# Kernel tuning notes

Hardware: AMD Instinct MI355X
Metric: run time of the kernel (lower is better)

The kernel has to match this reference:

```python
import jax, jax.numpy as jnp
import numpy as np

B, T, D_IN, D_H1, D_H2, K = 8, 1024, 256, 1024, 1024, 9
EPS = 1e-12

def setup_inputs() -> dict:
    key = jax.random.key(0)
    ks = jax.random.split(key, 11)
    return {
        "x": jax.random.normal(ks[0], (B, T, D_IN), jnp.float32),
        "d_w": jax.random.normal(ks[1], (B, D_H1, 1, K), jnp.float32),
        "d_g": jax.random.uniform(ks[2], (B, D_H1), jnp.float32),
        "d_b": jax.random.normal(ks[3], (B, D_H1), jnp.float32) * 0.02,
        "p_w": jax.random.normal(ks[4], (B, D_H1, D_H2, 1), jnp.float32),
        "p_g": jax.random.uniform(ks[5], (B, D_H1), jnp.float32),
        "p_b": jax.random.normal(ks[6], (B, D_H2), jnp.float32) * 0.02,
        "w1_w": jax.random.normal(ks[7], (D_H1, D_IN), jnp.float32) / np.sqrt(D_IN),
        "w1_b": jnp.zeros((D_H1,), jnp.float32),
        "w2_w": jax.random.normal(ks[8], (D_IN, D_H2), jnp.float32) / np.sqrt(D_H2),
        "w2_b": jnp.zeros((D_IN,), jnp.float32),
    }

def _mish(v):
    return v * jnp.tanh(jax.nn.softplus(v))

def _wnorm(w, g):
    # F.normalize over channel dim 1, scaled by per-(batch,channel) gain g
    n = jnp.maximum(jnp.linalg.norm(w, axis=1, keepdims=True), EPS)
    return (w / n) * g[:, :, None, None]

def reference(x, d_w, d_g, d_b, p_w, p_g, p_b, w1_w, w1_b, w2_w, w2_b):
    residual = x
    # w_1: conv1x1 projection d_in -> d_hid1, channels-first [B, C, T]
    h = jnp.einsum('bti,ci->bct', x, w1_w) + w1_b[None, :, None]
    h = _mish(h)  # dropout is identity in eval
    k = d_w.shape[-1]
    p = (k - 1) // 2
    t = h.shape[-1]
    hp = jnp.pad(h, ((0, 0), (0, 0), (p, p)))
    # unfold: overlapping windows [B, C, T, K] (small fixed K loop)
    x_unf = jnp.stack([hp[:, :, i:i + t] for i in range(k)], axis=-1)
    dw = _wnorm(d_w, d_g)[:, :, 0, :]  # [B, C, K]
    y = jnp.einsum('bctk,bck->bct', x_unf, dw) + d_b[:, :, None]
    pw = _wnorm(p_w, p_g)[..., 0]      # [B, C, O]
    y = jnp.einsum('bct,bco->bot', y, pw) + p_b[:, :, None]
    # w_2: conv1x1 projection d_hid2 -> d_in, back to [B, T, d_in]
    out = jnp.einsum('bot,io->bti', y, w2_w) + w2_b
    return out + residual
```

## Files before the change

kernel.cpp:

```cpp
#include <hip/hip_runtime.h>
#include <hip/hip_bf16.h>

#define B_  8
#define T_  1024
#define DI_ 256
#define C_  1024
#define O_  1024
#define KW  9
#define BT_ 8192
#define EPSF 1e-12f

typedef unsigned short u16;
typedef u16   ushort8 __attribute__((ext_vector_type(8)));
typedef u16   ushort4v __attribute__((ext_vector_type(4)));
typedef __bf16 bf16x8 __attribute__((ext_vector_type(8)));
typedef float  f32x4  __attribute__((ext_vector_type(4)));

#define GLOAD_LDS16(g, l) __builtin_amdgcn_global_load_lds( \
    (const __attribute__((address_space(1))) void*)(g),      \
    (__attribute__((address_space(3))) void*)(l), 16, 0, 0)

__device__ __forceinline__ float bf2f(u16 u) {
    union { unsigned int i; float f; } z; z.i = ((unsigned int)u) << 16; return z.f;
}
__device__ __forceinline__ u16 f2bf(float f) {
    union { float f; unsigned int i; } z; z.f = f;
    unsigned int i = z.i;
    i += 0x7FFFu + ((i >> 16) & 1u);
    return (u16)(i >> 16);
}
__device__ __forceinline__ float mishf(float v) {
    float u = __expf(v);
    float w = 1.f + u;
    return v * (1.f - 2.f / (w * w + 1.f));
}

#define PB_XB 2048
#define PB_W1 2304
#define PB_W2 2560
#define PB_DN 2568
#define PB_PT 4616

__global__ __launch_bounds__(256)
void prep_k(const float* __restrict__ x,   u16* __restrict__ xb,
            const float* __restrict__ w1w, u16* __restrict__ w1b16,
            const float* __restrict__ w2w, u16* __restrict__ w2b16,
            const float* __restrict__ d_w, const float* __restrict__ d_g,
            float* __restrict__ dwf,
            const float* __restrict__ p_w, const float* __restrict__ p_g,
            float* __restrict__ part, u16* __restrict__ pwT)
{
    const int bid = blockIdx.x;
    const int tid = threadIdx.x;

    if (bid < PB_W2) {
        const float* in;
        u16* out;
        int i;
        if (bid < PB_XB)      { in = x;   out = xb;    i = bid * 256 + tid; }
        else if (bid < PB_W1) { in = w1w; out = w1b16; i = (bid - PB_XB) * 256 + tid; }
        else                  { in = w2w; out = w2b16; i = (bid - PB_W1) * 256 + tid; }
        float4 v = ((const float4*)in)[i];
        ushort4v o;
        o.x = f2bf(v.x); o.y = f2bf(v.y); o.z = f2bf(v.z); o.w = f2bf(v.w);
        ((ushort4v*)out)[i] = o;
    } else if (bid < PB_DN) {
        __shared__ float red[KW][256];
        __shared__ float nrm[KW];
        const int b = bid - PB_W2;
        float s[KW];
#pragma unroll
        for (int k = 0; k < KW; k++) s[k] = 0.f;
        for (int c = tid; c < C_; c += 256) {
#pragma unroll
            for (int k = 0; k < KW; k++) {
                float v = d_w[((size_t)b * C_ + c) * KW + k];
                s[k] += v * v;
            }
        }
#pragma unroll
        for (int k = 0; k < KW; k++) red[k][tid] = s[k];
        __syncthreads();
        if (tid < KW) {
            float t = 0.f;
            for (int i = 0; i < 256; i++) t += red[tid][i];
            nrm[tid] = fmaxf(sqrtf(t), EPSF);
        }
        __syncthreads();
        for (int c = tid; c < C_; c += 256) {
            float g = d_g[(size_t)b * C_ + c];
#pragma unroll
            for (int k = 0; k < KW; k++)
                dwf[((size_t)b * C_ + c) * KW + k] =
                    d_w[((size_t)b * C_ + c) * KW + k] / nrm[k] * g;
        }
    } else {
        __shared__ float ts[64][65];
        __shared__ float sq[4][64];
        const int idx = bid - PB_DN;
        const int b   = idx >> 8;
        const int rem = idx & 255;
        const int c0  = (rem >> 4) * 64, o0 = (rem & 15) * 64;
        const int col = tid & 63;
        const int rg  = tid >> 6;
        float ssq = 0.f;
        for (int r = rg; r < 64; r += 4) {
            float v = p_w[((size_t)b * C_ + c0 + r) * O_ + o0 + col];
            ssq += v * v;
            ts[r][col] = v * p_g[(size_t)b * C_ + c0 + r];
        }
        sq[rg][col] = ssq;
        __syncthreads();
        if (tid < 64)
            part[((size_t)b * 16 + (rem >> 4)) * O_ + o0 + tid] =
                sq[0][tid] + sq[1][tid] + sq[2][tid] + sq[3][tid];
        for (int r = rg; r < 64; r += 4)
            pwT[((size_t)b * O_ + o0 + r) * C_ + c0 + col] = f2bf(ts[col][r]);
    }
}

__global__ __launch_bounds__(256)
void dwconv_k(const u16* __restrict__ h, const float* __restrict__ dwf,
              const float* __restrict__ d_b, u16* __restrict__ y1gT)
{
    __shared__ u16 hs[64][74];
    const int b  = blockIdx.z;
    const int c0 = blockIdx.y * 64, t0 = blockIdx.x * 64;
    const int tid = threadIdx.x;
    for (int idx = tid; idx < 64 * 72; idx += 256) {
        int cc = idx / 72, tt = idx % 72;
        int t = t0 + tt - 4;
        u16 v = 0;
        if (t >= 0 && t < T_) v = h[(size_t)(c0 + cc) * BT_ + b * T_ + t];
        hs[cc][tt] = v;
    }
    __syncthreads();
    const int cc = tid & 63;
    const int c  = c0 + cc;
    float w[KW];
#pragma unroll
    for (int k = 0; k < KW; k++) w[k] = dwf[((size_t)b * C_ + c) * KW + k];
    const float bb = d_b[(size_t)b * C_ + c];
    for (int tt = tid >> 6; tt < 64; tt += 4) {
        float s = bb;
#pragma unroll
        for (int k = 0; k < KW; k++) s += bf2f(hs[cc][tt + k]) * w[k];
        y1gT[((size_t)b * T_ + t0 + tt) * C_ + c] = f2bf(s);
    }
}

template<int EPI>
__device__ __forceinline__ void gemmw_body(
    const u16* __restrict__ A, const u16* __restrict__ Bt,
    u16* __restrict__ Db, const float* __restrict__ bias,
    const float* __restrict__ extra, int M, int N, int Kd)
{
    __shared__ u16 As[2][128 * 32];
    __shared__ u16 Bs[2][256 * 32];

    const int gx = gridDim.x;
    const unsigned nwg = (unsigned)gx * gridDim.y;
    unsigned lin = blockIdx.y * gx + blockIdx.x;
    lin = (lin & 7u) * (nwg >> 3) + (lin >> 3);
    const int m0 = (int)(lin / gx) * 128;
    const int n0 = (int)(lin % gx) * 256;

    const int b = (EPI == 1) ? (m0 >> 10) : 0;
    if (EPI == 1) {
        Bt    += (size_t)b * O_ * C_;
        bias  += (size_t)b * O_;
        extra += (size_t)b * 16 * O_;
    }

    const int tid  = threadIdx.x;
    const int lane = tid & 63, wave = tid >> 6;
    const int wm = (wave >> 1) * 64, wn = (wave & 1) * 128;
    const int lr = lane & 15;

    const int srow  = lane >> 2;
    const int scolE = ((lane & 3) ^ (srow & 3)) * 8;

    f32x4 acc[4][8];
#pragma unroll
    for (int i = 0; i < 4; i++)
#pragma unroll
        for (int j = 0; j < 8; j++) acc[i][j] = (f32x4){0.f, 0.f, 0.f, 0.f};

    auto STAGE = [&](int buf, int k0) {
#pragma unroll
        for (int i = 0; i < 2; i++)
            GLOAD_LDS16(&A[(size_t)(m0 + i * 64 + wave * 16 + srow) * Kd + k0 + scolE],
                        &As[buf][(i * 64 + wave * 16) * 32]);
#pragma unroll
        for (int i = 0; i < 4; i++)
            GLOAD_LDS16(&Bt[(size_t)(n0 + i * 64 + wave * 16 + srow) * Kd + k0 + scolE],
                        &Bs[buf][(i * 64 + wave * 16) * 32]);
    };

    const int NT = Kd >> 5;
    STAGE(0, 0);
    for (int kt = 0; kt < NT; kt++) {
        __syncthreads();
        if (kt + 1 < NT) STAGE((kt + 1) & 1, (kt + 1) << 5);
        const u16* as = As[kt & 1];
        const u16* bs = Bs[kt & 1];
        const int slot = lane >> 4;
        const int sw = (slot ^ (lr & 3)) << 3;
        bf16x8 av[4], bv[8];
#pragma unroll
        for (int i = 0; i < 4; i++)
            av[i] = *(const bf16x8*)&as[(wm + i * 16 + lr) * 32 + sw];
#pragma unroll
        for (int j = 0; j < 8; j++)
            bv[j] = *(const bf16x8*)&bs[(wn + j * 16 + lr) * 32 + sw];
#pragma unroll
        for (int i = 0; i < 4; i++)
#pragma unroll
            for (int j = 0; j < 8; j++)
                acc[i][j] = __builtin_amdgcn_mfma_f32_16x16x32_bf16(
                    av[i], bv[j], acc[i][j], 0, 0, 0);
    }

    const int r0 = (lane >> 4) * 4;
#pragma unroll
    for (int i = 0; i < 4; i++) {
#pragma unroll
        for (int j = 0; j < 8; j++) {
            const int col = n0 + wn + j * 16 + lr;
            float iv = 0.f;
            if (EPI == 1) {
                float s = 0.f;
#pragma unroll
                for (int ch = 0; ch < 16; ch++)
                    s += extra[(size_t)ch * O_ + col];
                iv = 1.f / fmaxf(sqrtf(s), EPSF);
            }
#pragma unroll
            for (int r = 0; r < 4; r++) {
                const int row = m0 + wm + i * 16 + r0 + r;
                float v = acc[i][j][r];
                if (EPI == 0) {
                    v += bias[row];
                    v = mishf(v);
                } else {
                    v = v * iv + bias[col];
                }
                Db[(size_t)row * N + col] = f2bf(v);
            }
        }
    }
}

__global__ __launch_bounds__(256, 1)
void gemm1_k(const u16* __restrict__ A, const u16* __restrict__ Bt,
             u16* __restrict__ D, const float* __restrict__ bias,
             int M, int N, int Kd)
{
    gemmw_body<0>(A, Bt, D, bias, nullptr, M, N, Kd);
}

__global__ __launch_bounds__(256, 1)
void gemm2_k(const u16* __restrict__ A, const u16* __restrict__ Bt,
             u16* __restrict__ D, const float* __restrict__ bias,
             const float* __restrict__ extra, int M, int N, int Kd)
{
    gemmw_body<1>(A, Bt, D, bias, extra, M, N, Kd);
}

__global__ __launch_bounds__(256)
void gemm3_k(const u16* __restrict__ A, const u16* __restrict__ Bt,
             float* __restrict__ Df, const float* __restrict__ bias,
             const float* __restrict__ X, int M, int N, int Kd)
{
    __shared__ u16 As[2][128 * 64];
    __shared__ u16 Bs[2][64 * 64];

    const int gx = gridDim.x;
    const unsigned nwg = (unsigned)gx * gridDim.y;
    unsigned lin = blockIdx.y * gx + blockIdx.x;
    lin = (lin & 7u) * (nwg >> 3) + (lin >> 3);
    const int m0 = (int)(lin / gx) * 128;
    const int n0 = (int)(lin % gx) * 64;

    const int tid  = threadIdx.x;
    const int lane = tid & 63, wave = tid >> 6;
    const int wm = (wave & 1) * 64, wn = (wave >> 1) * 32;
    const int lr = lane & 15;

    const int sbase = wave * 8;
    const int srowL = lane >> 3;
    const int scolE = ((lane & 7) ^ srowL) * 8;

    f32x4 acc[4][2];
#pragma unroll
    for (int i = 0; i < 4; i++)
#pragma unroll
        for (int j = 0; j < 2; j++) acc[i][j] = (f32x4){0.f, 0.f, 0.f, 0.f};

    auto STAGE = [&](int buf, int k0) {
#pragma unroll
        for (int i = 0; i < 4; i++)
            GLOAD_LDS16(&A[(size_t)(m0 + i * 32 + sbase + srowL) * Kd + k0 + scolE],
                        &As[buf][(i * 32 + sbase) * 64]);
#pragma unroll
        for (int i = 0; i < 2; i++)
            GLOAD_LDS16(&Bt[(size_t)(n0 + i * 32 + sbase + srowL) * Kd + k0 + scolE],
                        &Bs[buf][(i * 32 + sbase) * 64]);
    };

    const int NT = Kd >> 6;
    STAGE(0, 0);
    for (int kt = 0; kt < NT; kt++) {
        __syncthreads();
        if (kt + 1 < NT) STAGE((kt + 1) & 1, (kt + 1) << 6);
        const u16* as = As[kt & 1];
        const u16* bs = Bs[kt & 1];
        bf16x8 av[2][4], bv[2][2];
#pragma unroll
        for (int kk = 0; kk < 2; kk++) {
            const int slot = (lane >> 4) + kk * 4;
            const int sw = (slot ^ (lr & 7)) << 3;
#pragma unroll
            for (int i = 0; i < 4; i++)
                av[kk][i] = *(const bf16x8*)&as[(wm + i * 16 + lr) * 64 + sw];
#pragma unroll
            for (int j = 0; j < 2; j++)
                bv[kk][j] = *(const bf16x8*)&bs[(wn + j * 16 + lr) * 64 + sw];
        }
#pragma unroll
        for (int kk = 0; kk < 2; kk++)
#pragma unroll
            for (int i = 0; i < 4; i++)
#pragma unroll
                for (int j = 0; j < 2; j++)
                    acc[i][j] = __builtin_amdgcn_mfma_f32_16x16x32_bf16(
                        av[kk][i], bv[kk][j], acc[i][j], 0, 0, 0);
    }

    const int r0 = (lane >> 4) * 4;
#pragma unroll
    for (int i = 0; i < 4; i++) {
#pragma unroll
        for (int j = 0; j < 2; j++) {
            const int col = n0 + wn + j * 16 + lr;
#pragma unroll
            for (int r = 0; r < 4; r++) {
                const int row = m0 + wm + i * 16 + r0 + r;
                Df[(size_t)row * N + col] =
                    acc[i][j][r] + bias[col] + X[(size_t)row * N + col];
            }
        }
    }
}

extern "C" void kernel_launch(void* const* d_in, const int* in_sizes, int n_in,
                              void* d_out, int out_size, void* d_ws, size_t ws_size,
                              hipStream_t stream)
{
    const float* x   = (const float*)d_in[0];
    const float* d_w = (const float*)d_in[1];
    const float* d_g = (const float*)d_in[2];
    const float* d_b = (const float*)d_in[3];
    const float* p_w = (const float*)d_in[4];
    const float* p_g = (const float*)d_in[5];
    const float* p_b = (const float*)d_in[6];
    const float* w1w = (const float*)d_in[7];
    const float* w1b = (const float*)d_in[8];
    const float* w2w = (const float*)d_in[9];
    const float* w2b = (const float*)d_in[10];
    float* out = (float*)d_out;

    char* ws = (char*)d_ws;
    const size_t SZ = (size_t)16777216;
    u16*   h    = (u16*)(ws);
    u16*   y1gT = (u16*)(ws + SZ);
    u16*   pwT  = (u16*)(ws + 2 * SZ);
    u16*   y2T  = (u16*)(ws + 3 * SZ);
    u16*   xb   = (u16*)(ws + 4 * SZ);
    u16*   w1b16= (u16*)(ws + 4 * SZ + 4194304);
    u16*   w2b16= (u16*)(ws + 4 * SZ + 4718592);
    float* dwf  = (float*)(ws + 4 * SZ + 5242880);
    float* part = (float*)(ws + 4 * SZ + 5242880 + 294912);

    prep_k<<<dim3(PB_PT), 256, 0, stream>>>(
        x, xb, w1w, w1b16, w2w, w2b16, d_w, d_g, dwf, p_w, p_g, part, pwT);

    gemm1_k<<<dim3(BT_ / 256, C_ / 128), 256, 0, stream>>>(
        w1b16, xb, h, w1b, C_, BT_, DI_);

    dwconv_k<<<dim3(T_ / 64, C_ / 64, B_), 256, 0, stream>>>(h, dwf, d_b, y1gT);

    gemm2_k<<<dim3(O_ / 256, BT_ / 128), 256, 0, stream>>>(
        y1gT, pwT, y2T, p_b, part, BT_, O_, C_);

    gemm3_k<<<dim3(DI_ / 64, BT_ / 128), 256, 0, stream>>>(
        y2T, w2b16, out, w2b, x, BT_, DI_, O_);
}
```

Measured before the change: 119.0 us.

## Triple-buffer GEMM pipelines with 8-wave tiles and smaller gemm3 blocks

The two large GEMMs (w1 projection and pointwise conv) move from 4 waves per 128x256 tile with a double-buffered K=32 stage to 8 waves with a triple-buffered K=64 stage. The per-iteration __syncthreads is replaced by a partial vmcnt wait plus s_barrier, and MFMA blocks are wrapped in s_setprio so load latency overlaps compute. The final GEMM shrinks to 64x64 tiles on 2 waves with triple-buffered K=32 stages, which raises block count and occupancy. This costs more LDS per block (144 KB for gemm1/2, from 48 KB) and relies on hand-counted vmcnt values being correct.

```diff
diff --git a/kernel.cpp b/kernel.cpp
--- a/kernel.cpp
+++ b/kernel.cpp
@@ -150,13 +150,13 @@
 }
 
 template<int EPI>
-__device__ __forceinline__ void gemmw_body(
+__device__ __forceinline__ void gemm12_body(
     const u16* __restrict__ A, const u16* __restrict__ Bt,
     u16* __restrict__ Db, const float* __restrict__ bias,
     const float* __restrict__ extra, int M, int N, int Kd)
 {
-    __shared__ u16 As[2][128 * 32];
-    __shared__ u16 Bs[2][256 * 32];
+    __shared__ u16 As[3 * 128 * 64];
+    __shared__ u16 Bs[3 * 256 * 64];
 
     const int gx = gridDim.x;
     const unsigned nwg = (unsigned)gx * gridDim.y;
@@ -174,58 +174,74 @@
 
     const int tid  = threadIdx.x;
     const int lane = tid & 63, wave = tid >> 6;
-    const int wm = (wave >> 1) * 64, wn = (wave & 1) * 128;
+    const int wm = (wave >> 2) * 64, wn = (wave & 3) * 64;
     const int lr = lane & 15;
-
-    const int srow  = lane >> 2;
-    const int scolE = ((lane & 3) ^ (srow & 3)) * 8;
-
-    f32x4 acc[4][8];
+    const int srow8 = tid >> 3;
+    const int scolE = ((tid & 7) ^ ((tid >> 3) & 7)) * 8;
+
+    f32x4 acc[4][4];
 #pragma unroll
     for (int i = 0; i < 4; i++)
 #pragma unroll
-        for (int j = 0; j < 8; j++) acc[i][j] = (f32x4){0.f, 0.f, 0.f, 0.f};
-
-    auto STAGE = [&](int buf, int k0) {
+        for (int j = 0; j < 4; j++) acc[i][j] = (f32x4){0.f, 0.f, 0.f, 0.f};
+
+    auto STAGE = [&](int buf, int kt) {
+        const int k0 = kt << 6;
 #pragma unroll
         for (int i = 0; i < 2; i++)
-            GLOAD_LDS16(&A[(size_t)(m0 + i * 64 + wave * 16 + srow) * Kd + k0 + scolE],
-                        &As[buf][(i * 64 + wave * 16) * 32]);
+            GLOAD_LDS16(&A[(size_t)(m0 + i * 64 + srow8) * Kd + k0 + scolE],
+                        &As[buf * 8192 + (i * 64 + wave * 8) * 64]);
 #pragma unroll
         for (int i = 0; i < 4; i++)
-            GLOAD_LDS16(&Bt[(size_t)(n0 + i * 64 + wave * 16 + srow) * Kd + k0 + scolE],
-                        &Bs[buf][(i * 64 + wave * 16) * 32]);
+            GLOAD_LDS16(&Bt[(size_t)(n0 + i * 64 + srow8) * Kd + k0 + scolE],
+                        &Bs[buf * 16384 + (i * 64 + wave * 8) * 64]);
     };
 
-    const int NT = Kd >> 5;
+    const int NT = Kd >> 6;
     STAGE(0, 0);
+    STAGE(1, 1);
+    int rb = 0, sb = 2;
     for (int kt = 0; kt < NT; kt++) {
-        __syncthreads();
-        if (kt + 1 < NT) STAGE((kt + 1) & 1, (kt + 1) << 5);
-        const u16* as = As[kt & 1];
-        const u16* bs = Bs[kt & 1];
-        const int slot = lane >> 4;
-        const int sw = (slot ^ (lr & 3)) << 3;
-        bf16x8 av[4], bv[8];
-#pragma unroll
-        for (int i = 0; i < 4; i++)
-            av[i] = *(const bf16x8*)&as[(wm + i * 16 + lr) * 32 + sw];
-#pragma unroll
-        for (int j = 0; j < 8; j++)
-            bv[j] = *(const bf16x8*)&bs[(wn + j * 16 + lr) * 32 + sw];
-#pragma unroll
-        for (int i = 0; i < 4; i++)
-#pragma unroll
-            for (int j = 0; j < 8; j++)
-                acc[i][j] = __builtin_amdgcn_mfma_f32_16x16x32_bf16(
-                    av[i], bv[j], acc[i][j], 0, 0, 0);
+        if (kt == NT - 1) {
+            asm volatile("s_waitcnt vmcnt(0)" ::: "memory");
+        } else {
+            asm volatile("s_waitcnt vmcnt(6)" ::: "memory");
+        }
+        __builtin_amdgcn_s_barrier();
+        if (kt + 2 < NT) STAGE(sb, kt + 2);
+        const u16* as = &As[rb * 8192];
+        const u16* bs = &Bs[rb * 16384];
+        bf16x8 av[2][4], bv[2][4];
+#pragma unroll
+        for (int kk = 0; kk < 2; kk++) {
+            const int q  = (lane >> 4) + kk * 4;
+            const int sw = (q ^ (lr & 7)) << 3;
+#pragma unroll
+            for (int i = 0; i < 4; i++)
+                av[kk][i] = *(const bf16x8*)&as[(wm + i * 16 + lr) * 64 + sw];
+#pragma unroll
+            for (int j = 0; j < 4; j++)
+                bv[kk][j] = *(const bf16x8*)&bs[(wn + j * 16 + lr) * 64 + sw];
+        }
+        __builtin_amdgcn_s_setprio(1);
+#pragma unroll
+        for (int kk = 0; kk < 2; kk++)
+#pragma unroll
+            for (int i = 0; i < 4; i++)
+#pragma unroll
+                for (int j = 0; j < 4; j++)
+                    acc[i][j] = __builtin_amdgcn_mfma_f32_16x16x32_bf16(
+                        av[kk][i], bv[kk][j], acc[i][j], 0, 0, 0);
+        __builtin_amdgcn_s_setprio(0);
+        rb = (rb == 2) ? 0 : rb + 1;
+        sb = (sb == 2) ? 0 : sb + 1;
     }
 
     const int r0 = (lane >> 4) * 4;
 #pragma unroll
     for (int i = 0; i < 4; i++) {
 #pragma unroll
-        for (int j = 0; j < 8; j++) {
+        for (int j = 0; j < 4; j++) {
             const int col = n0 + wn + j * 16 + lr;
             float iv = 0.f;
             if (EPI == 1) {
@@ -251,45 +267,45 @@
     }
 }
 
-__global__ __launch_bounds__(256, 1)
+__global__ __launch_bounds__(512, 2)
 void gemm1_k(const u16* __restrict__ A, const u16* __restrict__ Bt,
              u16* __restrict__ D, const float* __restrict__ bias,
              int M, int N, int Kd)
 {
-    gemmw_body<0>(A, Bt, D, bias, nullptr, M, N, Kd);
-}
-
-__global__ __launch_bounds__(256, 1)
+    gemm12_body<0>(A, Bt, D, bias, nullptr, M, N, Kd);
+}
+
+__global__ __launch_bounds__(512, 2)
 void gemm2_k(const u16* __restrict__ A, const u16* __restrict__ Bt,
              u16* __restrict__ D, const float* __restrict__ bias,
              const float* __restrict__ extra, int M, int N, int Kd)
 {
-    gemmw_body<1>(A, Bt, D, bias, extra, M, N, Kd);
-}
-
-__global__ __launch_bounds__(256)
+    gemm12_body<1>(A, Bt, D, bias, extra, M, N, Kd);
+}
+
+__global__ __launch_bounds__(128, 2)
 void gemm3_k(const u16* __restrict__ A, const u16* __restrict__ Bt,
              float* __restrict__ Df, const float* __restrict__ bias,
              const float* __restrict__ X, int M, int N, int Kd)
 {
-    __shared__ u16 As[2][128 * 64];
-    __shared__ u16 Bs[2][64 * 64];
+    __shared__ u16 As[3 * 2048];
+    __shared__ u16 Bs[3 * 2048];
 
     const int gx = gridDim.x;
     const unsigned nwg = (unsigned)gx * gridDim.y;
     unsigned lin = blockIdx.y * gx + blockIdx.x;
     lin = (lin & 7u) * (nwg >> 3) + (lin >> 3);
-    const int m0 = (int)(lin / gx) * 128;
+    const int m0 = (int)(lin / gx) * 64;
     const int n0 = (int)(lin % gx) * 64;
 
     const int tid  = threadIdx.x;
     const int lane = tid & 63, wave = tid >> 6;
-    const int wm = (wave & 1) * 64, wn = (wave >> 1) * 32;
+    const int wn = wave * 32;
     const int lr = lane & 15;
-
-    const int sbase = wave * 8;
-    const int srowL = lane >> 3;
-    const int scolE = ((lane & 7) ^ srowL) * 8;
+    const int q  = lane >> 4;
+    const int srow  = lane >> 2;
+    const int scolE = ((lane & 3) ^ ((lane >> 3) & 3)) * 8;
+    const int sw    = (q ^ ((lr >> 1) & 3)) << 3;
 
     f32x4 acc[4][2];
 #pragma unroll
@@ -297,44 +313,49 @@
 #pragma unroll
         for (int j = 0; j < 2; j++) acc[i][j] = (f32x4){0.f, 0.f, 0.f, 0.f};
 
-    auto STAGE = [&](int buf, int k0) {
+    auto STAGE = [&](int buf, int kt) {
+        const int k0 = kt << 5;
+#pragma unroll
+        for (int i = 0; i < 2; i++)
+            GLOAD_LDS16(&A[(size_t)(m0 + wave * 32 + i * 16 + srow) * Kd + k0 + scolE],
+                        &As[buf * 2048 + (wave * 32 + i * 16) * 32]);
+#pragma unroll
+        for (int i = 0; i < 2; i++)
+            GLOAD_LDS16(&Bt[(size_t)(n0 + wave * 32 + i * 16 + srow) * Kd + k0 + scolE],
+                        &Bs[buf * 2048 + (wave * 32 + i * 16) * 32]);
+    };
+
+    const int NT = Kd >> 5;
+    STAGE(0, 0);
+    STAGE(1, 1);
+    int rb = 0, sb = 2;
+    for (int kt = 0; kt < NT; kt++) {
+        if (kt == NT - 1) {
+            asm volatile("s_waitcnt vmcnt(0)" ::: "memory");
+        } else {
+            asm volatile("s_waitcnt vmcnt(4)" ::: "memory");
+        }
+        __builtin_amdgcn_s_barrier();
+        if (kt + 2 < NT) STAGE(sb, kt + 2);
+        const u16* as = &As[rb * 2048];
+        const u16* bs = &Bs[rb * 2048];
+        bf16x8 av[4], bv[2];
 #pragma unroll
         for (int i = 0; i < 4; i++)
-            GLOAD_LDS16(&A[(size_t)(m0 + i * 32 + sbase + srowL) * Kd + k0 + scolE],
-                        &As[buf][(i * 32 + sbase) * 64]);
-#pragma unroll
-        for (int i = 0; i < 2; i++)
-            GLOAD_LDS16(&Bt[(size_t)(n0 + i * 32 + sbase + srowL) * Kd + k0 + scolE],
-                        &Bs[buf][(i * 32 + sbase) * 64]);
-    };
-
-    const int NT = Kd >> 6;
-    STAGE(0, 0);
-    for (int kt = 0; kt < NT; kt++) {
-        __syncthreads();
-        if (kt + 1 < NT) STAGE((kt + 1) & 1, (kt + 1) << 6);
-        const u16* as = As[kt & 1];
-        const u16* bs = Bs[kt & 1];
-        bf16x8 av[2][4], bv[2][2];
-#pragma unroll
-        for (int kk = 0; kk < 2; kk++) {
-            const int slot = (lane >> 4) + kk * 4;
-            const int sw = (slot ^ (lr & 7)) << 3;
-#pragma unroll
-            for (int i = 0; i < 4; i++)
-                av[kk][i] = *(const bf16x8*)&as[(wm + i * 16 + lr) * 64 + sw];
+            av[i] = *(const bf16x8*)&as[(i * 16 + lr) * 32 + sw];
+#pragma unroll
+        for (int j = 0; j < 2; j++)
+            bv[j] = *(const bf16x8*)&bs[(wn + j * 16 + lr) * 32 + sw];
+        __builtin_amdgcn_s_setprio(1);
+#pragma unroll
+        for (int i = 0; i < 4; i++)
 #pragma unroll
             for (int j = 0; j < 2; j++)
-                bv[kk][j] = *(const bf16x8*)&bs[(wn + j * 16 + lr) * 64 + sw];
-        }
-#pragma unroll
-        for (int kk = 0; kk < 2; kk++)
-#pragma unroll
-            for (int i = 0; i < 4; i++)
-#pragma unroll
-                for (int j = 0; j < 2; j++)
-                    acc[i][j] = __builtin_amdgcn_mfma_f32_16x16x32_bf16(
-                        av[kk][i], bv[kk][j], acc[i][j], 0, 0, 0);
+                acc[i][j] = __builtin_amdgcn_mfma_f32_16x16x32_bf16(
+                    av[i], bv[j], acc[i][j], 0, 0, 0);
+        __builtin_amdgcn_s_setprio(0);
+        rb = (rb == 2) ? 0 : rb + 1;
+        sb = (sb == 2) ? 0 : sb + 1;
     }
 
     const int r0 = (lane >> 4) * 4;
@@ -345,7 +366,7 @@
             const int col = n0 + wn + j * 16 + lr;
 #pragma unroll
             for (int r = 0; r < 4; r++) {
-                const int row = m0 + wm + i * 16 + r0 + r;
+                const int row = m0 + i * 16 + r0 + r;
                 Df[(size_t)row * N + col] =
                     acc[i][j][r] + bias[col] + X[(size_t)row * N + col];
             }
@@ -385,14 +406,14 @@
     prep_k<<<dim3(PB_PT), 256, 0, stream>>>(
         x, xb, w1w, w1b16, w2w, w2b16, d_w, d_g, dwf, p_w, p_g, part, pwT);
 
-    gemm1_k<<<dim3(BT_ / 256, C_ / 128), 256, 0, stream>>>(
+    gemm1_k<<<dim3(BT_ / 256, C_ / 128), 512, 0, stream>>>(
         w1b16, xb, h, w1b, C_, BT_, DI_);
 
     dwconv_k<<<dim3(T_ / 64, C_ / 64, B_), 256, 0, stream>>>(h, dwf, d_b, y1gT);
 
-    gemm2_k<<<dim3(O_ / 256, BT_ / 128), 256, 0, stream>>>(
+    gemm2_k<<<dim3(O_ / 256, BT_ / 128), 512, 0, stream>>>(
         y1gT, pwT, y2T, p_b, part, BT_, O_, C_);
 
-    gemm3_k<<<dim3(DI_ / 64, BT_ / 128), 256, 0, stream>>>(
+    gemm3_k<<<dim3(DI_ / 64, BT_ / 64), 128, 0, stream>>>(
         y2T, w2b16, out, w2b, x, BT_, DI_, O_);
 }
```

Result: faster. 104.0 us (-12.6%).
